# Kernel optimization log

Hardware: AMD Instinct MI355X
Metric: run time of the kernel (lower is better)

The kernel has to match this reference:

```python
import math
import jax, jax.numpy as jnp
import numpy as np

B, N, DIN, DOUT = 64, 512, 256, 256
EPS = 1e-5  # torch BatchNorm1d default


def setup_inputs() -> dict:
    key = jax.random.key(0)
    k0, k1, k2, k3 = jax.random.split(key, 4)
    x = jax.random.normal(k0, (B, N, DIN), dtype=jnp.float32)
    # row-scaled dense adjacency (keeps activation magnitudes sane)
    adj = jax.random.uniform(k1, (B, N, N), dtype=jnp.float32) / N
    # prefix-style masks: first L_i nodes of each graph are valid
    lengths = jax.random.randint(k2, (B,), N // 4, N + 1)
    mask = (jnp.arange(N)[None, :] < lengths[:, None]).astype(jnp.float32)
    # xavier_normal_ init for weight
    std = math.sqrt(2.0 / (DIN + DOUT))
    weight = jax.random.normal(k3, (DIN, DOUT), dtype=jnp.float32) * std
    bias = jnp.zeros((DOUT,), dtype=jnp.float32)
    gamma = jnp.ones((DOUT,), dtype=jnp.float32)   # BN affine scale
    beta = jnp.zeros((DOUT,), dtype=jnp.float32)   # BN affine shift
    return {"x": x, "adj": adj, "mask": mask, "weight": weight,
            "bias": bias, "gamma": gamma, "beta": beta}


def reference(x, adj, mask, weight, bias, gamma, beta):
    # y = adj @ x @ W + b
    y = jnp.einsum('bnm,bmd->bnd', adj, x)
    y = jnp.einsum('bnd,de->bne', y, weight) + bias
    # masked BatchNorm1d (training mode): batch stats over all valid nodes,
    # equivalent to the torch code's pack -> BN -> unpack on prefix masks.
    m = mask[:, :, None]                       # [B, N, 1]
    n = jnp.sum(mask)                          # total valid nodes
    mean = jnp.sum(y * m, axis=(0, 1)) / n     # [DOUT]
    var = jnp.sum(((y - mean) ** 2) * m, axis=(0, 1)) / n  # biased var
    y = ((y - mean) * jax.lax.rsqrt(var + EPS) * gamma + beta) * m
    return jax.nn.relu(y)
```

## Files before the change

kernel.cpp:

```cpp
#include <hip/hip_runtime.h>

#define B_    64
#define N_    512
#define DIN_  256
#define DOUT_ 256
#define EPS_  1e-5f
#define ROWS_ (B_ * N_)
#define NBLK_Y2 512

typedef __attribute__((ext_vector_type(8))) short bf16x8;
typedef __attribute__((ext_vector_type(4))) float f32x4;
typedef __attribute__((ext_vector_type(4))) short short4v;

__device__ __forceinline__ short f2bf(float f) {
    unsigned u = __builtin_bit_cast(unsigned, f);
    u += 0x7fff + ((u >> 16) & 1);
    return (short)(u >> 16);
}

__device__ __forceinline__ void gload_lds16(const void* g, void* l) {
    __builtin_amdgcn_global_load_lds(
        (const __attribute__((address_space(1))) void*)g,
        (__attribute__((address_space(3))) void*)l, 16, 0, 0);
}


__global__ __launch_bounds__(256) void wt_cvt(const float* __restrict__ W,
                                              short* __restrict__ WTf) {
    const int c = blockIdx.x * 256 + threadIdx.x;
    const int kf = c >> 10, ef = (c >> 6) & 15, lp = c & 63;
    const int e = ef * 16 + (lp & 15);
    const int k0 = kf * 32 + (lp >> 4) * 8;
    bf16x8 h;
    #pragma unroll
    for (int j = 0; j < 8; ++j)
        h[j] = f2bf(W[(size_t)(k0 + j) * DOUT_ + e]);
    *(bf16x8*)&WTf[(size_t)c * 8] = h;
}

__global__ __launch_bounds__(512, 4) void gemm_xw(const float* __restrict__ X,
                                                  const short* __restrict__ WTf,
                                                  short* __restrict__ xwT) {
    __shared__ __align__(16) short Bs[2][16384];
    __shared__ __align__(16) short As[2][4096];
    const int tid = threadIdx.x, wv = tid >> 6, lane = tid & 63;
    const int lrow = lane & 15, lg = lane >> 4;
    const int bid = blockIdx.x;
    const int rowBase = bid * 64;

    const int s_row = ((tid >> 6) & 3) * 16 + (tid & 15);
    const int s_kloc = (tid >> 8) * 32 + ((tid >> 4) & 3) * 8;
    const float* Xr = &X[(size_t)(rowBase + s_row) * DIN_ + s_kloc];

    f32x4 acc[4][2] = {};
    float4 av0, av1;

    av0 = *(const float4*)(Xr);
    av1 = *(const float4*)(Xr + 4);
    #pragma unroll
    for (int j = 0; j < 4; ++j) {
        int o = tid * 16 + j * 8192;
        gload_lds16((const char*)WTf + o, (char*)&Bs[0][0] + o);
    }
    {
        bf16x8 h = { f2bf(av0.x), f2bf(av0.y), f2bf(av0.z), f2bf(av0.w),
                     f2bf(av1.x), f2bf(av1.y), f2bf(av1.z), f2bf(av1.w) };
        *(bf16x8*)((char*)&As[0][0] + tid * 16) = h;
    }
    __syncthreads();

    int cur = 0;
    for (int c = 0; c < 4; ++c) {
        if (c < 3) {
            av0 = *(const float4*)(Xr + (c + 1) * 64);
            av1 = *(const float4*)(Xr + (c + 1) * 64 + 4);
            #pragma unroll
            for (int j = 0; j < 4; ++j) {
                int o = tid * 16 + j * 8192;
                gload_lds16((const char*)WTf + (c + 1) * 32768 + o,
                            (char*)&Bs[cur ^ 1][0] + o);
            }
        }
        #pragma unroll
        for (int kf2 = 0; kf2 < 2; ++kf2) {
            bf16x8 a[4], b[2];
            #pragma unroll
            for (int m = 0; m < 4; ++m)
                a[m] = *(const bf16x8*)((char*)&As[cur][0] +
                                        ((kf2 * 4 + m) * 64 + lane) * 16);
            #pragma unroll
            for (int nf = 0; nf < 2; ++nf)
                b[nf] = *(const bf16x8*)((char*)&Bs[cur][0] +
                                         ((kf2 * 16 + wv * 2 + nf) * 64 + lane) * 16);
            #pragma unroll
            for (int m = 0; m < 4; ++m)
                #pragma unroll
                for (int nf = 0; nf < 2; ++nf)
                    acc[m][nf] = __builtin_amdgcn_mfma_f32_16x16x32_bf16(
                        a[m], b[nf], acc[m][nf], 0, 0, 0);
        }
        if (c < 3) {
            bf16x8 h = { f2bf(av0.x), f2bf(av0.y), f2bf(av0.z), f2bf(av0.w),
                         f2bf(av1.x), f2bf(av1.y), f2bf(av1.z), f2bf(av1.w) };
            *(bf16x8*)((char*)&As[cur ^ 1][0] + tid * 16) = h;
        }
        __syncthreads();
        cur ^= 1;
    }

    const int bz = bid >> 3, kfbase = (bid & 7) * 2;
    short* xwb = xwT + (size_t)bz * 131072;
    #pragma unroll
    for (int m = 0; m < 4; ++m)
        #pragma unroll
        for (int nf = 0; nf < 2; ++nf) {
            int kf = kfbase + (m >> 1);
            int ef = wv * 2 + nf;
            int lanep = lrow + 16 * ((m & 1) * 2 + (lg >> 1));
            size_t off = ((size_t)(kf * 16 + ef) * 64 + lanep) * 8 + (lg & 1) * 4;
            short4v o = { f2bf(acc[m][nf][0]), f2bf(acc[m][nf][1]),
                          f2bf(acc[m][nf][2]), f2bf(acc[m][nf][3]) };
            *(short4v*)&xwb[off] = o;
        }
}

__global__ __launch_bounds__(512, 4) void gemm_y2(const float* __restrict__ adj,
                                                  const short* __restrict__ xwT,
                                                  const float* __restrict__ bias,
                                                  const float* __restrict__ mask,
                                                  float* __restrict__ y2,
                                                  float* __restrict__ psum,
                                                  float* __restrict__ psumsq,
                                                  float* __restrict__ pcnt) {
    __shared__ __align__(16) short Bs[2][16384];
    __shared__ __align__(16) short As[2][4096];
    const int tid = threadIdx.x, wv = tid >> 6, lane = tid & 63;
    const int lrow = lane & 15, lg = lane >> 4;
    const int bid = blockIdx.x;
    const int swz = ((bid & 7) << 6) | (bid >> 3);
    const int bz = swz >> 3, mt = swz & 7;
    const int rowBase = mt * 64;
    const float* A = adj + (size_t)bz * N_ * N_;
    const short* xwb = xwT + (size_t)bz * 131072;

    const int s_row = ((tid >> 6) & 3) * 16 + (tid & 15);
    const int s_kloc = (tid >> 8) * 32 + ((tid >> 4) & 3) * 8;
    const float* Ar = &A[(size_t)(rowBase + s_row) * N_ + s_kloc];

    f32x4 acc[4][2] = {};
    float4 av0, av1;

    av0 = *(const float4*)(Ar);
    av1 = *(const float4*)(Ar + 4);
    #pragma unroll
    for (int j = 0; j < 4; ++j) {
        int o = tid * 16 + j * 8192;
        gload_lds16((const char*)xwb + o, (char*)&Bs[0][0] + o);
    }
    {
        bf16x8 h = { f2bf(av0.x), f2bf(av0.y), f2bf(av0.z), f2bf(av0.w),
                     f2bf(av1.x), f2bf(av1.y), f2bf(av1.z), f2bf(av1.w) };
        *(bf16x8*)((char*)&As[0][0] + tid * 16) = h;
    }
    __syncthreads();

    int cur = 0;
    for (int c = 0; c < 8; ++c) {
        if (c < 7) {
            av0 = *(const float4*)(Ar + (c + 1) * 64);
            av1 = *(const float4*)(Ar + (c + 1) * 64 + 4);
            #pragma unroll
            for (int j = 0; j < 4; ++j) {
                int o = tid * 16 + j * 8192;
                gload_lds16((const char*)xwb + (c + 1) * 32768 + o,
                            (char*)&Bs[cur ^ 1][0] + o);
            }
        }
        #pragma unroll
        for (int kf2 = 0; kf2 < 2; ++kf2) {
            bf16x8 a[4], b[2];
            #pragma unroll
            for (int m = 0; m < 4; ++m)
                a[m] = *(const bf16x8*)((char*)&As[cur][0] +
                                        ((kf2 * 4 + m) * 64 + lane) * 16);
            #pragma unroll
            for (int nf = 0; nf < 2; ++nf)
                b[nf] = *(const bf16x8*)((char*)&Bs[cur][0] +
                                         ((kf2 * 16 + wv * 2 + nf) * 64 + lane) * 16);
            #pragma unroll
            for (int m = 0; m < 4; ++m)
                #pragma unroll
                for (int nf = 0; nf < 2; ++nf)
                    acc[m][nf] = __builtin_amdgcn_mfma_f32_16x16x32_bf16(
                        a[m], b[nf], acc[m][nf], 0, 0, 0);
        }
        if (c < 7) {
            bf16x8 h = { f2bf(av0.x), f2bf(av0.y), f2bf(av0.z), f2bf(av0.w),
                         f2bf(av1.x), f2bf(av1.y), f2bf(av1.z), f2bf(av1.w) };
            *(bf16x8*)((char*)&As[cur ^ 1][0] + tid * 16) = h;
        }
        __syncthreads();
        cur ^= 1;
    }

    float* C = y2 + (size_t)bz * N_ * DOUT_;
    float mv[4][4];
    #pragma unroll
    for (int m = 0; m < 4; ++m)
        #pragma unroll
        for (int r = 0; r < 4; ++r)
            mv[m][r] = mask[bz * N_ + rowBase + m * 16 + lg * 4 + r];
    float sv[2] = {0.f, 0.f}, sq[2] = {0.f, 0.f};
    #pragma unroll
    for (int nf = 0; nf < 2; ++nf) {
        const int col = wv * 32 + nf * 16 + lrow;
        const float bv = bias[col];
        #pragma unroll
        for (int m = 0; m < 4; ++m) {
            const int r0 = rowBase + m * 16 + lg * 4;
            #pragma unroll
            for (int r = 0; r < 4; ++r) {
                float v = acc[m][nf][r] + bv;
                C[(size_t)(r0 + r) * DOUT_ + col] = v;
                float vm = v * mv[m][r];
                sv[nf] += vm;
                sq[nf] = fmaf(v, vm, sq[nf]);
            }
        }
    }
    #pragma unroll
    for (int nf = 0; nf < 2; ++nf) {
        sv[nf] += __shfl_xor(sv[nf], 16); sv[nf] += __shfl_xor(sv[nf], 32);
        sq[nf] += __shfl_xor(sq[nf], 16); sq[nf] += __shfl_xor(sq[nf], 32);
    }
    const int pidx = bz * 8 + mt;
    if (lg == 0) {
        #pragma unroll
        for (int nf = 0; nf < 2; ++nf) {
            psum[(size_t)pidx * DOUT_ + wv * 32 + nf * 16 + lrow]   = sv[nf];
            psumsq[(size_t)pidx * DOUT_ + wv * 32 + nf * 16 + lrow] = sq[nf];
        }
    }
    if (wv == 0) {
        float cnt = mask[bz * N_ + rowBase + lane];
        #pragma unroll
        for (int i = 1; i < 64; i <<= 1) cnt += __shfl_xor(cnt, i);
        if (lane == 0) pcnt[pidx] = cnt;
    }
}

__global__ __launch_bounds__(256) void finalize2(const float* __restrict__ psum,
                                                 const float* __restrict__ psumsq,
                                                 const float* __restrict__ pcnt,
                                                 const float* __restrict__ gamma,
                                                 const float* __restrict__ beta,
                                                 float* __restrict__ scsh) {
    const int e = blockIdx.x, t = threadIdx.x;
    float s  = psum[(size_t)t * DOUT_ + e]   + psum[(size_t)(t + 256) * DOUT_ + e];
    float ss = psumsq[(size_t)t * DOUT_ + e] + psumsq[(size_t)(t + 256) * DOUT_ + e];
    float n  = pcnt[t] + pcnt[t + 256];
    #pragma unroll
    for (int i = 1; i < 64; i <<= 1) {
        s += __shfl_xor(s, i); ss += __shfl_xor(ss, i); n += __shfl_xor(n, i);
    }
    __shared__ float red[3][4];
    const int wv = t >> 6;
    if ((t & 63) == 0) { red[0][wv] = s; red[1][wv] = ss; red[2][wv] = n; }
    __syncthreads();
    if (t == 0) {
        s  = red[0][0] + red[0][1] + red[0][2] + red[0][3];
        ss = red[1][0] + red[1][1] + red[1][2] + red[1][3];
        n  = red[2][0] + red[2][1] + red[2][2] + red[2][3];
        float mean = s / n;
        float var = ss / n - mean * mean;
        float sc = rsqrtf(var + EPS_) * gamma[e];
        scsh[e] = sc;
        scsh[DOUT_ + e] = beta[e] - mean * sc;
    }
}

__global__ __launch_bounds__(256) void norm_relu(float* __restrict__ y2,
                                                 const float* __restrict__ mask,
                                                 const float* __restrict__ scsh) {
    const int nq = ROWS_ * (DOUT_ / 4);
    for (int q = blockIdx.x * blockDim.x + threadIdx.x; q < nq;
         q += gridDim.x * blockDim.x) {
        int e4 = (q & 63) * 4;
        int r = q >> 6;
        float m = mask[r];
        float4 v  = *(float4*)&y2[(size_t)q * 4];
        float4 sc = *(const float4*)&scsh[e4];
        float4 sh = *(const float4*)&scsh[DOUT_ + e4];
        v.x = fmaxf(fmaf(v.x, sc.x, sh.x) * m, 0.f);
        v.y = fmaxf(fmaf(v.y, sc.y, sh.y) * m, 0.f);
        v.z = fmaxf(fmaf(v.z, sc.z, sh.z) * m, 0.f);
        v.w = fmaxf(fmaf(v.w, sc.w, sh.w) * m, 0.f);
        *(float4*)&y2[(size_t)q * 4] = v;
    }
}

extern "C" void kernel_launch(void* const* d_in, const int* in_sizes, int n_in,
                              void* d_out, int out_size, void* d_ws, size_t ws_size,
                              hipStream_t stream) {
    const float* x      = (const float*)d_in[0];
    const float* adj    = (const float*)d_in[1];
    const float* mask   = (const float*)d_in[2];
    const float* weight = (const float*)d_in[3];
    const float* bias   = (const float*)d_in[4];
    const float* gamma  = (const float*)d_in[5];
    const float* beta   = (const float*)d_in[6];
    float* out = (float*)d_out;

    short* WTf    = (short*)d_ws;
    short* xwT    = WTf + 256 * 256;
    float* psum   = (float*)(xwT + (size_t)DOUT_ * ROWS_);
    float* psumsq = psum + NBLK_Y2 * DOUT_;
    float* pcnt   = psumsq + NBLK_Y2 * DOUT_;
    float* scsh   = pcnt + NBLK_Y2;

    wt_cvt<<<32, 256, 0, stream>>>(weight, WTf);
    gemm_xw<<<512, 512, 0, stream>>>(x, WTf, xwT);
    gemm_y2<<<512, 512, 0, stream>>>(adj, xwT, bias, mask, out, psum, psumsq, pcnt);
    finalize2<<<256, 256, 0, stream>>>(psum, psumsq, pcnt, gamma, beta, scsh);
    norm_relu<<<2048, 256, 0, stream>>>(out, mask, scsh);
}
```

Measured before the change: 55.99 us.

## Deepen gemm_y2 pipeline with 4-stage B ring and store bf16 intermediate

```diff
diff --git a/kernel.cpp b/kernel.cpp
--- a/kernel.cpp
+++ b/kernel.cpp
@@ -9,6 +9,7 @@
 #define NBLK_Y2 512
 
 typedef __attribute__((ext_vector_type(8))) short bf16x8;
+typedef __attribute__((ext_vector_type(8))) unsigned short u16x8;
 typedef __attribute__((ext_vector_type(4))) float f32x4;
 typedef __attribute__((ext_vector_type(4))) short short4v;
 
@@ -124,16 +125,18 @@
         }
 }
 
+template <bool BF16Y2>
 __global__ __launch_bounds__(512, 4) void gemm_y2(const float* __restrict__ adj,
                                                   const short* __restrict__ xwT,
                                                   const float* __restrict__ bias,
                                                   const float* __restrict__ mask,
-                                                  float* __restrict__ y2,
+                                                  float* __restrict__ outf,
+                                                  unsigned short* __restrict__ y2b,
                                                   float* __restrict__ psum,
                                                   float* __restrict__ psumsq,
                                                   float* __restrict__ pcnt) {
-    __shared__ __align__(16) short Bs[2][16384];
-    __shared__ __align__(16) short As[2][4096];
+    __shared__ __align__(16) short Bs[4][8192];
+    __shared__ __align__(16) short As[2][2048];
     const int tid = threadIdx.x, wv = tid >> 6, lane = tid & 63;
     const int lrow = lane & 15, lg = lane >> 4;
     const int bid = blockIdx.x;
@@ -143,67 +146,84 @@
     const float* A = adj + (size_t)bz * N_ * N_;
     const short* xwb = xwT + (size_t)bz * 131072;
 
-    const int s_row = ((tid >> 6) & 3) * 16 + (tid & 15);
-    const int s_kloc = (tid >> 8) * 32 + ((tid >> 4) & 3) * 8;
-    const float* Ar = &A[(size_t)(rowBase + s_row) * N_ + s_kloc];
-
+    const int arow = ((tid >> 7) << 4) | ((tid >> 1) & 15);
+    const int akl  = (((tid >> 5) & 3) << 3) | ((tid & 1) << 2);
+    const float* Ar = &A[(size_t)(rowBase + arow) * N_ + akl];
+
+    float4 av[2];
     f32x4 acc[4][2] = {};
-    float4 av0, av1;
-
-    av0 = *(const float4*)(Ar);
-    av1 = *(const float4*)(Ar + 4);
-    #pragma unroll
-    for (int j = 0; j < 4; ++j) {
-        int o = tid * 16 + j * 8192;
-        gload_lds16((const char*)xwb + o, (char*)&Bs[0][0] + o);
-    }
+
+    float4 av0t = *(const float4*)(Ar);
+    av[1] = *(const float4*)(Ar + 32);
+    __builtin_amdgcn_sched_barrier(0);
+    #pragma unroll
+    for (int p = 0; p < 3; ++p) {
+        const char* src = (const char*)xwb + p * 16384;
+        char* dst = (char*)&Bs[p][0];
+        gload_lds16(src + tid * 16, dst + tid * 16);
+        gload_lds16(src + tid * 16 + 8192, dst + tid * 16 + 8192);
+    }
+    __builtin_amdgcn_sched_barrier(0);
     {
-        bf16x8 h = { f2bf(av0.x), f2bf(av0.y), f2bf(av0.z), f2bf(av0.w),
-                     f2bf(av1.x), f2bf(av1.y), f2bf(av1.z), f2bf(av1.w) };
-        *(bf16x8*)((char*)&As[0][0] + tid * 16) = h;
-    }
-    __syncthreads();
-
-    int cur = 0;
-    for (int c = 0; c < 8; ++c) {
-        if (c < 7) {
-            av0 = *(const float4*)(Ar + (c + 1) * 64);
-            av1 = *(const float4*)(Ar + (c + 1) * 64 + 4);
-            #pragma unroll
-            for (int j = 0; j < 4; ++j) {
-                int o = tid * 16 + j * 8192;
-                gload_lds16((const char*)xwb + (c + 1) * 32768 + o,
-                            (char*)&Bs[cur ^ 1][0] + o);
-            }
-        }
-        #pragma unroll
-        for (int kf2 = 0; kf2 < 2; ++kf2) {
-            bf16x8 a[4], b[2];
-            #pragma unroll
-            for (int m = 0; m < 4; ++m)
-                a[m] = *(const bf16x8*)((char*)&As[cur][0] +
-                                        ((kf2 * 4 + m) * 64 + lane) * 16);
-            #pragma unroll
-            for (int nf = 0; nf < 2; ++nf)
-                b[nf] = *(const bf16x8*)((char*)&Bs[cur][0] +
-                                         ((kf2 * 16 + wv * 2 + nf) * 64 + lane) * 16);
-            #pragma unroll
-            for (int m = 0; m < 4; ++m)
-                #pragma unroll
-                for (int nf = 0; nf < 2; ++nf)
-                    acc[m][nf] = __builtin_amdgcn_mfma_f32_16x16x32_bf16(
-                        a[m], b[nf], acc[m][nf], 0, 0, 0);
-        }
-        if (c < 7) {
-            bf16x8 h = { f2bf(av0.x), f2bf(av0.y), f2bf(av0.z), f2bf(av0.w),
-                         f2bf(av1.x), f2bf(av1.y), f2bf(av1.z), f2bf(av1.w) };
-            *(bf16x8*)((char*)&As[cur ^ 1][0] + tid * 16) = h;
-        }
-        __syncthreads();
-        cur ^= 1;
-    }
-
-    float* C = y2 + (size_t)bz * N_ * DOUT_;
+        short4v h = { f2bf(av0t.x), f2bf(av0t.y), f2bf(av0t.z), f2bf(av0t.w) };
+        *(short4v*)((char*)&As[0][0] + tid * 8) = h;
+    }
+    asm volatile("s_waitcnt lgkmcnt(0)" ::: "memory");
+    asm volatile("s_waitcnt vmcnt(4)" ::: "memory");
+    __builtin_amdgcn_s_barrier();
+    asm volatile("" ::: "memory");
+
+    #pragma unroll 1
+    for (int cc = 0; cc < 16; cc += 4) {
+        #pragma unroll
+        for (int u = 0; u < 4; ++u) {
+            const int c = cc + u;
+            {
+                const int cn = (c + 2 < 16) ? c + 2 : 15;
+                av[c & 1] = *(const float4*)(Ar + cn * 32);
+            }
+            __builtin_amdgcn_sched_barrier(0);
+            {
+                const int cn = (c + 3 < 16) ? c + 3 : 15;
+                const char* src = (const char*)xwb + cn * 16384;
+                char* dst = (char*)&Bs[(c + 3) & 3][0];
+                gload_lds16(src + tid * 16, dst + tid * 16);
+                gload_lds16(src + tid * 16 + 8192, dst + tid * 16 + 8192);
+            }
+            __builtin_amdgcn_sched_barrier(0);
+            {
+                const char* ab = (const char*)&As[c & 1][0];
+                const char* bb = (const char*)&Bs[c & 3][0];
+                bf16x8 a0 = *(const bf16x8*)(ab + (0 * 64 + lane) * 16);
+                bf16x8 a1 = *(const bf16x8*)(ab + (1 * 64 + lane) * 16);
+                bf16x8 a2 = *(const bf16x8*)(ab + (2 * 64 + lane) * 16);
+                bf16x8 a3 = *(const bf16x8*)(ab + (3 * 64 + lane) * 16);
+                bf16x8 b0 = *(const bf16x8*)(bb + ((wv * 2 + 0) * 64 + lane) * 16);
+                bf16x8 b1 = *(const bf16x8*)(bb + ((wv * 2 + 1) * 64 + lane) * 16);
+                acc[0][0] = __builtin_amdgcn_mfma_f32_16x16x32_bf16(a0, b0, acc[0][0], 0, 0, 0);
+                acc[0][1] = __builtin_amdgcn_mfma_f32_16x16x32_bf16(a0, b1, acc[0][1], 0, 0, 0);
+                acc[1][0] = __builtin_amdgcn_mfma_f32_16x16x32_bf16(a1, b0, acc[1][0], 0, 0, 0);
+                acc[1][1] = __builtin_amdgcn_mfma_f32_16x16x32_bf16(a1, b1, acc[1][1], 0, 0, 0);
+                acc[2][0] = __builtin_amdgcn_mfma_f32_16x16x32_bf16(a2, b0, acc[2][0], 0, 0, 0);
+                acc[2][1] = __builtin_amdgcn_mfma_f32_16x16x32_bf16(a2, b1, acc[2][1], 0, 0, 0);
+                acc[3][0] = __builtin_amdgcn_mfma_f32_16x16x32_bf16(a3, b0, acc[3][0], 0, 0, 0);
+                acc[3][1] = __builtin_amdgcn_mfma_f32_16x16x32_bf16(a3, b1, acc[3][1], 0, 0, 0);
+            }
+            __builtin_amdgcn_sched_barrier(0);
+            {
+                float4 v = av[(c + 1) & 1];
+                short4v h = { f2bf(v.x), f2bf(v.y), f2bf(v.z), f2bf(v.w) };
+                *(short4v*)((char*)&As[(c + 1) & 1][0] + tid * 8) = h;
+            }
+            asm volatile("s_waitcnt lgkmcnt(0)" ::: "memory");
+            asm volatile("s_waitcnt vmcnt(5)" ::: "memory");
+            __builtin_amdgcn_s_barrier();
+            asm volatile("" ::: "memory");
+        }
+    }
+
+    float* C = outf + (size_t)bz * N_ * DOUT_;
+    unsigned short* Cb = y2b + (size_t)bz * N_ * DOUT_;
     float mv[4][4];
     #pragma unroll
     for (int m = 0; m < 4; ++m)
@@ -221,7 +241,10 @@
             #pragma unroll
             for (int r = 0; r < 4; ++r) {
                 float v = acc[m][nf][r] + bv;
-                C[(size_t)(r0 + r) * DOUT_ + col] = v;
+                if (BF16Y2)
+                    Cb[(size_t)(r0 + r) * DOUT_ + col] = (unsigned short)f2bf(v);
+                else
+                    C[(size_t)(r0 + r) * DOUT_ + col] = v;
                 float vm = v * mv[m][r];
                 sv[nf] += vm;
                 sq[nf] = fmaf(v, vm, sq[nf]);
@@ -279,9 +302,40 @@
     }
 }
 
-__global__ __launch_bounds__(256) void norm_relu(float* __restrict__ y2,
-                                                 const float* __restrict__ mask,
-                                                 const float* __restrict__ scsh) {
+__global__ __launch_bounds__(256) void norm_relu_bf(const unsigned short* __restrict__ y2b,
+                                                    const float* __restrict__ mask,
+                                                    const float* __restrict__ scsh,
+                                                    float* __restrict__ out) {
+    const int nq = ROWS_ * (DOUT_ / 8);
+    for (int q = blockIdx.x * blockDim.x + threadIdx.x; q < nq;
+         q += gridDim.x * blockDim.x) {
+        int e8 = (q & 31) * 8;
+        int r = q >> 5;
+        float m = mask[r];
+        u16x8 uv = *(const u16x8*)&y2b[(size_t)q * 8];
+        float4 sc0 = *(const float4*)&scsh[e8];
+        float4 sc1 = *(const float4*)&scsh[e8 + 4];
+        float4 sh0 = *(const float4*)&scsh[DOUT_ + e8];
+        float4 sh1 = *(const float4*)&scsh[DOUT_ + e8 + 4];
+        float4 o0, o1;
+        #pragma unroll
+        for (int j = 0; j < 4; ++j) {
+            float f = __builtin_bit_cast(float, (unsigned)uv[j] << 16);
+            (&o0.x)[j] = fmaxf(fmaf(f, (&sc0.x)[j], (&sh0.x)[j]) * m, 0.f);
+        }
+        #pragma unroll
+        for (int j = 0; j < 4; ++j) {
+            float f = __builtin_bit_cast(float, (unsigned)uv[j + 4] << 16);
+            (&o1.x)[j] = fmaxf(fmaf(f, (&sc1.x)[j], (&sh1.x)[j]) * m, 0.f);
+        }
+        *(float4*)&out[(size_t)q * 8] = o0;
+        *(float4*)&out[(size_t)q * 8 + 4] = o1;
+    }
+}
+
+__global__ __launch_bounds__(256) void norm_relu_f32(float* __restrict__ y2,
+                                                     const float* __restrict__ mask,
+                                                     const float* __restrict__ scsh) {
     const int nq = ROWS_ * (DOUT_ / 4);
     for (int q = blockIdx.x * blockDim.x + threadIdx.x; q < nq;
          q += gridDim.x * blockDim.x) {
@@ -311,16 +365,30 @@
     const float* beta   = (const float*)d_in[6];
     float* out = (float*)d_out;
 
+    const size_t xw_elems = (size_t)DOUT_ * ROWS_;
+    const size_t need_bf = 131072 + xw_elems * 2 * 2 +
+                           (size_t)NBLK_Y2 * DOUT_ * 4 * 2 + NBLK_Y2 * 4 + 2048 + 64;
+    const bool use_bf = ws_size >= need_bf;
+
     short* WTf    = (short*)d_ws;
     short* xwT    = WTf + 256 * 256;
-    float* psum   = (float*)(xwT + (size_t)DOUT_ * ROWS_);
+    unsigned short* y2b = (unsigned short*)(xwT + xw_elems);
+    float* psum   = use_bf ? (float*)(y2b + xw_elems) : (float*)(y2b);
     float* psumsq = psum + NBLK_Y2 * DOUT_;
     float* pcnt   = psumsq + NBLK_Y2 * DOUT_;
     float* scsh   = pcnt + NBLK_Y2;
 
     wt_cvt<<<32, 256, 0, stream>>>(weight, WTf);
     gemm_xw<<<512, 512, 0, stream>>>(x, WTf, xwT);
-    gemm_y2<<<512, 512, 0, stream>>>(adj, xwT, bias, mask, out, psum, psumsq, pcnt);
-    finalize2<<<256, 256, 0, stream>>>(psum, psumsq, pcnt, gamma, beta, scsh);
-    norm_relu<<<2048, 256, 0, stream>>>(out, mask, scsh);
-}
+    if (use_bf) {
+        gemm_y2<true><<<NBLK_Y2, 512, 0, stream>>>(adj, xwT, bias, mask, out, y2b,
+                                                   psum, psumsq, pcnt);
+        finalize2<<<256, 256, 0, stream>>>(psum, psumsq, pcnt, gamma, beta, scsh);
+        norm_relu_bf<<<2048, 256, 0, stream>>>(y2b, mask, scsh, out);
+    } else {
+        gemm_y2<false><<<NBLK_Y2, 512, 0, stream>>>(adj, xwT, bias, mask, out, y2b,
+                                                    psum, psumsq, pcnt);
+        finalize2<<<256, 256, 0, stream>>>(psum, psumsq, pcnt, gamma, beta, scsh);
+        norm_relu_f32<<<2048, 256, 0, stream>>>(out, mask, scsh);
+    }
+}
```

Result: no change. 55.20 us (-1.4%).
